# Optimization experiments

Hardware: AMD Instinct MI355X
Metric: run time of the kernel (lower is better)

## Reference

```python
import jax, jax.numpy as jnp
import numpy as np

IN_F = 8192
OUT_F = 8192
BATCH = 16

def setup_inputs() -> dict:
    key = jax.random.key(0)
    k_x, k_q, k_s, k_b = jax.random.split(key, 4)
    x = jax.random.normal(k_x, (BATCH, IN_F), dtype=jnp.float32)
    # symmetric int4: values in [-8, 7]
    qweight = jax.random.randint(k_q, (OUT_F, IN_F), -8, 8, dtype=jnp.int32)
    scale = jax.random.uniform(k_s, (), dtype=jnp.float32) * 0.05 + 1e-3
    bias = jax.random.normal(k_b, (OUT_F,), dtype=jnp.float32)
    return {"x": x, "qweight": qweight, "scale": scale, "bias": bias}

def reference(x, qweight, scale, bias):
    # F.linear(x, qweight.float() * scale, bias)
    # Factor scale out of the GEMM: (x @ (q*s).T) == (x @ q.T) * s
    acc = jnp.einsum('bi,oi->bo', x, qweight.astype(jnp.float32))
    return acc * scale + bias
```

## Files before the change

kernel.cpp:

```cpp
#include <hip/hip_runtime.h>
#include <hip/hip_bf16.h>

#define IN_F  8192
#define OUT_F 8192
#define BATCH 16
#define KSPLIT 8
#define KCHUNK (IN_F / KSPLIT)
#define NSTEPS (KCHUNK / 32)
#define THREADS 256
#define ROWS_PER_BLOCK 64
#define XPAD 8
#define XSTRIDE (KCHUNK + XPAD)

typedef __attribute__((ext_vector_type(8))) short bf16x8;
typedef __attribute__((ext_vector_type(4))) float f32x4;

__global__ __launch_bounds__(256)
void init_out_kernel(const float* __restrict__ bias, float* __restrict__ out)
{
    const int i = blockIdx.x * 256 + threadIdx.x;
    out[i] = bias[i & (OUT_F - 1)];
}

__global__ __launch_bounds__(THREADS, 4)
void gptq_mfma_kernel(const float* __restrict__ x,
                      const int*  __restrict__ qw,
                      const float* __restrict__ scale,
                      float* __restrict__ out)
{
    __shared__ __align__(16) unsigned short xs[BATCH][XSTRIDE];

    const int tid  = threadIdx.x;
    const int lane = tid & 63;
    const int wave = tid >> 6;
    const int mn   = lane & 15;
    const int kgrp = lane >> 4;
    const int kidx = blockIdx.x & (KSPLIT - 1);
    const int row0 = (blockIdx.x >> 3) * ROWS_PER_BLOCK + wave * 16;
    const int k0   = kidx * KCHUNK;

    #pragma unroll
    for (int r = 0; r < BATCH; ++r) {
        const float4 v = *reinterpret_cast<const float4*>(x + (size_t)r * IN_F + k0 + tid * 4);
        ushort4 p;
        p.x = __bfloat16_as_ushort(__float2bfloat16(v.x));
        p.y = __bfloat16_as_ushort(__float2bfloat16(v.y));
        p.z = __bfloat16_as_ushort(__float2bfloat16(v.z));
        p.w = __bfloat16_as_ushort(__float2bfloat16(v.w));
        *reinterpret_cast<ushort4*>(&xs[r][tid * 4]) = p;
    }
    __syncthreads();

    const int* qsrc = qw + (size_t)(row0 + mn) * IN_F + k0 + kgrp * 8;
    const unsigned short* asrc = &xs[mn][kgrp * 8];

    f32x4 acc = {0.f, 0.f, 0.f, 0.f};

    int4 bca = *reinterpret_cast<const int4*>(qsrc);
    int4 bcb = *reinterpret_cast<const int4*>(qsrc + 4);
    bf16x8 ac = *reinterpret_cast<const bf16x8*>(asrc);

    #pragma unroll 1
    for (int s = 0; s < NSTEPS; ++s) {
        int4 bna, bnb;
        bf16x8 an;
        const bool more = (s + 1 < NSTEPS);
        if (more) {
            bna = *reinterpret_cast<const int4*>(qsrc + (s + 1) * 32);
            bnb = *reinterpret_cast<const int4*>(qsrc + (s + 1) * 32 + 4);
            an  = *reinterpret_cast<const bf16x8*>(asrc + (s + 1) * 32);
        }

        bf16x8 bw;
        bw[0] = __bfloat16_as_short(__float2bfloat16((float)bca.x));
        bw[1] = __bfloat16_as_short(__float2bfloat16((float)bca.y));
        bw[2] = __bfloat16_as_short(__float2bfloat16((float)bca.z));
        bw[3] = __bfloat16_as_short(__float2bfloat16((float)bca.w));
        bw[4] = __bfloat16_as_short(__float2bfloat16((float)bcb.x));
        bw[5] = __bfloat16_as_short(__float2bfloat16((float)bcb.y));
        bw[6] = __bfloat16_as_short(__float2bfloat16((float)bcb.z));
        bw[7] = __bfloat16_as_short(__float2bfloat16((float)bcb.w));

        acc = __builtin_amdgcn_mfma_f32_16x16x32_bf16(ac, bw, acc, 0, 0, 0);

        if (more) { bca = bna; bcb = bnb; ac = an; }
    }

    const float sc = scale[0];
    float* obase = out + row0 + mn;
    #pragma unroll
    for (int v = 0; v < 4; ++v) {
        const int m = kgrp * 4 + v;
        atomicAdd(obase + (size_t)m * OUT_F, acc[v] * sc);
    }
}

extern "C" void kernel_launch(void* const* d_in, const int* in_sizes, int n_in,
                              void* d_out, int out_size, void* d_ws, size_t ws_size,
                              hipStream_t stream) {
    const float* x     = (const float*)d_in[0];
    const int*   qw    = (const int*)d_in[1];
    const float* scale = (const float*)d_in[2];
    const float* bias  = (const float*)d_in[3];
    float*       out   = (float*)d_out;

    init_out_kernel<<<(BATCH * OUT_F) / 256, 256, 0, stream>>>(bias, out);

    dim3 grid((OUT_F / ROWS_PER_BLOCK) * KSPLIT);
    gptq_mfma_kernel<<<grid, THREADS, 0, stream>>>(x, qw, scale, out);
}
```

Before: 54.71 us.

## Replace split-K atomics with workspace partials plus reduce kernel; deepen load prefetch

When the workspace is large enough, each split-K block writes its partial sums to a per-split slice of the workspace, and a separate reduce kernel then sums the slices and applies scale and bias. This replaces the bias-init kernel and the float atomics on the output. The main loop is also unrolled by two, so two steps of weight and activation loads are in flight at once. The cost is an extra 4 MB of workspace writes and reads, plus higher register pressure from the deeper prefetch.

```diff
diff --git a/kernel.cpp b/kernel.cpp
--- a/kernel.cpp
+++ b/kernel.cpp
@@ -11,6 +11,7 @@
 #define ROWS_PER_BLOCK 64
 #define XPAD 8
 #define XSTRIDE (KCHUNK + XPAD)
+#define WS_NEEDED ((size_t)KSPLIT * BATCH * OUT_F * 4)
 
 typedef __attribute__((ext_vector_type(8))) short bf16x8;
 typedef __attribute__((ext_vector_type(4))) float f32x4;
@@ -22,11 +23,34 @@
     out[i] = bias[i & (OUT_F - 1)];
 }
 
+__global__ __launch_bounds__(256)
+void reduce_kernel(const float* __restrict__ ws,
+                   const float* __restrict__ scale,
+                   const float* __restrict__ bias,
+                   float* __restrict__ out)
+{
+    const int idx = (blockIdx.x * 256 + threadIdx.x) * 4;
+    const int o   = idx & (OUT_F - 1);
+    float4 s = {0.f, 0.f, 0.f, 0.f};
+    #pragma unroll
+    for (int k = 0; k < KSPLIT; ++k) {
+        const float4 p = *reinterpret_cast<const float4*>(ws + (size_t)k * BATCH * OUT_F + idx);
+        s.x += p.x; s.y += p.y; s.z += p.z; s.w += p.w;
+    }
+    const float sc = scale[0];
+    const float4 bv = *reinterpret_cast<const float4*>(bias + o);
+    float4 r;
+    r.x = s.x * sc + bv.x; r.y = s.y * sc + bv.y;
+    r.z = s.z * sc + bv.z; r.w = s.w * sc + bv.w;
+    *reinterpret_cast<float4*>(out + idx) = r;
+}
+
+template<bool USE_WS>
 __global__ __launch_bounds__(THREADS, 4)
 void gptq_mfma_kernel(const float* __restrict__ x,
                       const int*  __restrict__ qw,
                       const float* __restrict__ scale,
-                      float* __restrict__ out)
+                      float* __restrict__ dst)
 {
     __shared__ __align__(16) unsigned short xs[BATCH][XSTRIDE];
 
@@ -56,42 +80,64 @@
 
     f32x4 acc = {0.f, 0.f, 0.f, 0.f};
 
-    int4 bca = *reinterpret_cast<const int4*>(qsrc);
-    int4 bcb = *reinterpret_cast<const int4*>(qsrc + 4);
-    bf16x8 ac = *reinterpret_cast<const bf16x8*>(asrc);
+    int4 c0a = *reinterpret_cast<const int4*>(qsrc);
+    int4 c0b = *reinterpret_cast<const int4*>(qsrc + 4);
+    bf16x8 a0 = *reinterpret_cast<const bf16x8*>(asrc);
+    int4 c1a = *reinterpret_cast<const int4*>(qsrc + 32);
+    int4 c1b = *reinterpret_cast<const int4*>(qsrc + 36);
+    bf16x8 a1 = *reinterpret_cast<const bf16x8*>(asrc + 32);
 
     #pragma unroll 1
-    for (int s = 0; s < NSTEPS; ++s) {
-        int4 bna, bnb;
-        bf16x8 an;
-        const bool more = (s + 1 < NSTEPS);
-        if (more) {
-            bna = *reinterpret_cast<const int4*>(qsrc + (s + 1) * 32);
-            bnb = *reinterpret_cast<const int4*>(qsrc + (s + 1) * 32 + 4);
-            an  = *reinterpret_cast<const bf16x8*>(asrc + (s + 1) * 32);
+    for (int s = 0; s < NSTEPS; s += 2) {
+        int4 n0a, n0b, n1a, n1b;
+        bf16x8 na0, na1;
+        const bool m0 = (s + 2 < NSTEPS);
+        const bool m1 = (s + 3 < NSTEPS);
+        if (m0) {
+            n0a = *reinterpret_cast<const int4*>(qsrc + (s + 2) * 32);
+            n0b = *reinterpret_cast<const int4*>(qsrc + (s + 2) * 32 + 4);
+            na0 = *reinterpret_cast<const bf16x8*>(asrc + (s + 2) * 32);
+        }
+        if (m1) {
+            n1a = *reinterpret_cast<const int4*>(qsrc + (s + 3) * 32);
+            n1b = *reinterpret_cast<const int4*>(qsrc + (s + 3) * 32 + 4);
+            na1 = *reinterpret_cast<const bf16x8*>(asrc + (s + 3) * 32);
         }
 
         bf16x8 bw;
-        bw[0] = __bfloat16_as_short(__float2bfloat16((float)bca.x));
-        bw[1] = __bfloat16_as_short(__float2bfloat16((float)bca.y));
-        bw[2] = __bfloat16_as_short(__float2bfloat16((float)bca.z));
-        bw[3] = __bfloat16_as_short(__float2bfloat16((float)bca.w));
-        bw[4] = __bfloat16_as_short(__float2bfloat16((float)bcb.x));
-        bw[5] = __bfloat16_as_short(__float2bfloat16((float)bcb.y));
-        bw[6] = __bfloat16_as_short(__float2bfloat16((float)bcb.z));
-        bw[7] = __bfloat16_as_short(__float2bfloat16((float)bcb.w));
+        bw[0] = __bfloat16_as_short(__float2bfloat16((float)c0a.x));
+        bw[1] = __bfloat16_as_short(__float2bfloat16((float)c0a.y));
+        bw[2] = __bfloat16_as_short(__float2bfloat16((float)c0a.z));
+        bw[3] = __bfloat16_as_short(__float2bfloat16((float)c0a.w));
+        bw[4] = __bfloat16_as_short(__float2bfloat16((float)c0b.x));
+        bw[5] = __bfloat16_as_short(__float2bfloat16((float)c0b.y));
+        bw[6] = __bfloat16_as_short(__float2bfloat16((float)c0b.z));
+        bw[7] = __bfloat16_as_short(__float2bfloat16((float)c0b.w));
+        acc = __builtin_amdgcn_mfma_f32_16x16x32_bf16(a0, bw, acc, 0, 0, 0);
 
-        acc = __builtin_amdgcn_mfma_f32_16x16x32_bf16(ac, bw, acc, 0, 0, 0);
+        bw[0] = __bfloat16_as_short(__float2bfloat16((float)c1a.x));
+        bw[1] = __bfloat16_as_short(__float2bfloat16((float)c1a.y));
+        bw[2] = __bfloat16_as_short(__float2bfloat16((float)c1a.z));
+        bw[3] = __bfloat16_as_short(__float2bfloat16((float)c1a.w));
+        bw[4] = __bfloat16_as_short(__float2bfloat16((float)c1b.x));
+        bw[5] = __bfloat16_as_short(__float2bfloat16((float)c1b.y));
+        bw[6] = __bfloat16_as_short(__float2bfloat16((float)c1b.z));
+        bw[7] = __bfloat16_as_short(__float2bfloat16((float)c1b.w));
+        acc = __builtin_amdgcn_mfma_f32_16x16x32_bf16(a1, bw, acc, 0, 0, 0);
 
-        if (more) { bca = bna; bcb = bnb; ac = an; }
+        if (m0) { c0a = n0a; c0b = n0b; a0 = na0; }
+        if (m1) { c1a = n1a; c1b = n1b; a1 = na1; }
     }
 
     const float sc = scale[0];
-    float* obase = out + row0 + mn;
     #pragma unroll
     for (int v = 0; v < 4; ++v) {
         const int m = kgrp * 4 + v;
-        atomicAdd(obase + (size_t)m * OUT_F, acc[v] * sc);
+        if (USE_WS) {
+            dst[(size_t)kidx * BATCH * OUT_F + (size_t)m * OUT_F + row0 + mn] = acc[v];
+        } else {
+            atomicAdd(dst + (size_t)m * OUT_F + row0 + mn, acc[v] * sc);
+        }
     }
 }
 
@@ -103,9 +149,15 @@
     const float* scale = (const float*)d_in[2];
     const float* bias  = (const float*)d_in[3];
     float*       out   = (float*)d_out;
-
-    init_out_kernel<<<(BATCH * OUT_F) / 256, 256, 0, stream>>>(bias, out);
+    float*       ws    = (float*)d_ws;
 
     dim3 grid((OUT_F / ROWS_PER_BLOCK) * KSPLIT);
-    gptq_mfma_kernel<<<grid, THREADS, 0, stream>>>(x, qw, scale, out);
+
+    if (ws_size >= WS_NEEDED) {
+        gptq_mfma_kernel<true><<<grid, THREADS, 0, stream>>>(x, qw, scale, ws);
+        reduce_kernel<<<(BATCH * OUT_F) / 4 / 256, 256, 0, stream>>>(ws, scale, bias, out);
+    } else {
+        init_out_kernel<<<(BATCH * OUT_F) / 256, 256, 0, stream>>>(bias, out);
+        gptq_mfma_kernel<false><<<grid, THREADS, 0, stream>>>(x, qw, scale, out);
+    }
 }
```

Result: faster. 52.65 us (-3.8%).
